# Kernel optimization log

Measured on AMD Instinct MI355X. Metric: run time of the kernel, lower is better.

The kernel has to match this reference:

```python
import jax, jax.numpy as jnp
import numpy as np

LN_EPS = 1e-5


def _layer_norm(x, scale, bias):
    mu = jnp.mean(x, axis=-1, keepdims=True)
    var = jnp.mean(jnp.square(x - mu), axis=-1, keepdims=True)
    return (x - mu) * jax.lax.rsqrt(var + LN_EPS) * scale + bias


def setup_inputs() -> dict:
    key = jax.random.key(0)
    B, N, C_Z, C_H = 1, 512, 128, 128
    ks = jax.random.split(key, 8)
    s = 1.0 / np.sqrt(C_Z)
    inp = {
        "z": jax.random.normal(ks[0], (B, N, N, C_Z), dtype=jnp.float32),
        "mask": jnp.ones((B, N, N), dtype=jnp.float32),
        # gated / plain projections from c_z -> c_hidden
        "w_a_p": jax.random.normal(ks[1], (C_Z, C_H), dtype=jnp.float32) * s,
        "b_a_p": jnp.zeros((C_H,), dtype=jnp.float32),
        "w_a_g": jnp.zeros((C_Z, C_H), dtype=jnp.float32),  # gating init: zeros, bias ones
        "b_a_g": jnp.ones((C_H,), dtype=jnp.float32),
        "w_b_p": jax.random.normal(ks[2], (C_Z, C_H), dtype=jnp.float32) * s,
        "b_b_p": jnp.zeros((C_H,), dtype=jnp.float32),
        "w_b_g": jnp.zeros((C_Z, C_H), dtype=jnp.float32),
        "b_b_g": jnp.ones((C_H,), dtype=jnp.float32),
        # output gate c_z -> c_z (gating init)
        "w_g": jnp.zeros((C_Z, C_Z), dtype=jnp.float32),
        "b_g": jnp.ones((C_Z,), dtype=jnp.float32),
        # final projection c_hidden -> c_z ('final' init: zeros; use small randn for a nontrivial test)
        "w_z": jax.random.normal(ks[3], (C_H, C_Z), dtype=jnp.float32) * (1.0 / np.sqrt(C_H)),
        "b_z": jnp.zeros((C_Z,), dtype=jnp.float32),
        "ln_in_scale": jnp.ones((C_Z,), dtype=jnp.float32),
        "ln_in_bias": jnp.zeros((C_Z,), dtype=jnp.float32),
        "ln_out_scale": jnp.ones((C_H,), dtype=jnp.float32),
        "ln_out_bias": jnp.zeros((C_H,), dtype=jnp.float32),
    }
    return inp


def reference(z, mask, w_a_p, b_a_p, w_a_g, b_a_g, w_b_p, b_b_p, w_b_g, b_b_g,
              w_g, b_g, w_z, b_z, ln_in_scale, ln_in_bias, ln_out_scale, ln_out_bias):
    # tmu_type == 'outgoing'
    z = _layer_norm(z, ln_in_scale, ln_in_bias)          # [B,N,N,Cz]
    m = mask[..., None]                                   # [B,N,N,1]
    a = jax.nn.sigmoid(z @ w_a_g + b_a_g) * m * (z @ w_a_p + b_a_p)  # [B,N,N,Ch]
    b = jax.nn.sigmoid(z @ w_b_g + b_b_g) * m * (z @ w_b_p + b_b_p)  # [B,N,N,Ch]
    # outgoing: p[b,i,j,c] = sum_k a[b,i,k,c] * b[b,j,k,c]
    x = jnp.einsum("bikc,bjkc->bijc", a, b)              # [B,N,N,Ch]
    x = _layer_norm(x, ln_out_scale, ln_out_bias)
    x = x @ w_z + b_z                                    # [B,N,N,Cz]
    g = jax.nn.sigmoid(z @ w_g + b_g)                    # [B,N,N,Cz]
    return x * g
```

## Files before the change

### kernel.cpp

```cpp
#include <hip/hip_runtime.h>

typedef __attribute__((ext_vector_type(8))) short short8;
typedef __attribute__((ext_vector_type(4))) short short4v;
typedef __attribute__((ext_vector_type(4))) float float4v;
typedef __attribute__((ext_vector_type(2))) unsigned int uint2v;

#define NDIM 512
#define NN (NDIM*NDIM)
#define CD 128

__device__ __forceinline__ unsigned short f2b(float f) {
  union { float f; unsigned u; } v; v.f = f;
  unsigned r = v.u + 0x7FFFu + ((v.u >> 16) & 1u);
  return (unsigned short)(r >> 16);
}
__device__ __forceinline__ float b2f(unsigned short h) {
  union { unsigned u; float f; } v; v.u = ((unsigned)h) << 16; return v.f;
}
__device__ __forceinline__ float sigmoidf_(float x) { return 1.f / (1.f + __expf(-x)); }
__device__ __forceinline__ unsigned pk2(float a, float b) {
  return (unsigned)f2b(a) | ((unsigned)f2b(b) << 16);
}
__device__ __forceinline__ float4v mfma16(short8 a, short8 b, float4v c) {
  return __builtin_amdgcn_mfma_f32_16x16x32_bf16(a, b, c, 0, 0, 0);
}
__device__ __forceinline__ void gl_lds16(const short* g, short* l) {
  __builtin_amdgcn_global_load_lds(
      (const __attribute__((address_space(1))) unsigned int*)g,
      (__attribute__((address_space(3))) unsigned int*)l, 16, 0, 0);
}

__device__ __forceinline__ short8 fragr(const short* buf, int row, int j) {
  return *(const short8*)(buf + row * 128 + ((j ^ (row & 15)) << 3));
}

__device__ __forceinline__ void stageW(const short* wslot, short* sW, int t) {
#pragma unroll
  for (int i = 0; i < 8; ++i) {
    int U = i * 256 + t;
    int row = U >> 4, u = U & 15;
    gl_lds16(wslot + row * 128 + ((u ^ (row & 15)) << 3), sW + U * 8);
  }
}

__global__ __launch_bounds__(256) void kPrepW(
    const float* __restrict__ w0, const float* __restrict__ w1,
    const float* __restrict__ w2, const float* __restrict__ w3,
    const float* __restrict__ w4, short* __restrict__ wt)
{
  const int wi = blockIdx.y;
  const float* W = wi==0 ? w0 : wi==1 ? w1 : wi==2 ? w2 : wi==3 ? w3 : w4;
  const int e = blockIdx.x * 256 + threadIdx.x;
  const int k = e >> 7, n = e & 127;
  wt[wi * 16384 + n * 128 + k] = (short)f2b(W[k * CD + n]);
}

__global__ __launch_bounds__(256, 2) void kProj(
    const float* __restrict__ z, const float* __restrict__ mask,
    const short* __restrict__ wT,
    const float* __restrict__ b_a_p, const float* __restrict__ b_a_g,
    const float* __restrict__ b_b_p, const float* __restrict__ b_b_g,
    const float* __restrict__ b_g,
    const float* __restrict__ ln_s, const float* __restrict__ ln_b,
    short* __restrict__ a_t, short* __restrict__ b_t, short* __restrict__ g_out)
{
  __shared__ short zln[128 * 128];
  __shared__ short sW[128 * 128];
  const int t = threadIdx.x;
  const int r0 = blockIdx.x * 128;
  const int w = t >> 6, l = t & 63, lr = l & 15, lg = l >> 4;

  stageW(wT + 1 * 16384, sW, t);

#pragma unroll
  for (int h = 0; h < 2; ++h) {
    const int row = h * 64 + (t >> 2), q = t & 3;
    const float* zp = z + (size_t)(r0 + row) * CD + q * 32;
    float x[32];
#pragma unroll
    for (int i = 0; i < 8; ++i) {
      float4v v = *(const float4v*)(zp + i * 4);
#pragma unroll
      for (int e = 0; e < 4; ++e) x[i*4+e] = v[e];
    }
    float s = 0.f;
#pragma unroll
    for (int i = 0; i < 32; ++i) s += x[i];
    s += __shfl_xor(s, 1, 64);
    s += __shfl_xor(s, 2, 64);
    const float mu = s * (1.f/128.f);
    float vs = 0.f;
#pragma unroll
    for (int i = 0; i < 32; ++i) { float d = x[i]-mu; vs += d*d; }
    vs += __shfl_xor(vs, 1, 64);
    vs += __shfl_xor(vs, 2, 64);
    const float rstd = rsqrtf(vs * (1.f/128.f) + 1e-5f);
#pragma unroll
    for (int i = 0; i < 32; ++i) {
      int c = q*32 + i;
      float y = (x[i]-mu)*rstd*ln_s[c] + ln_b[c];
      zln[row*128 + (((c>>3) ^ (row & 15)) << 3) + (c & 7)] = (short)f2b(y);
    }
  }

  float bga[8], bpa[8], bgb[8], bpb[8];
#pragma unroll
  for (int cf = 0; cf < 8; ++cf) {
    bga[cf] = b_a_g[cf*16+lr]; bpa[cf] = b_a_p[cf*16+lr];
    bgb[cf] = b_b_g[cf*16+lr]; bpb[cf] = b_b_p[cf*16+lr];
  }
  float mrow[2][4];
#pragma unroll
  for (int g = 0; g < 2; ++g)
#pragma unroll
    for (int jj = 0; jj < 4; ++jj)
      mrow[g][jj] = mask[r0 + w*32 + g*16 + lg*4 + jj];

  __syncthreads();

  short8 af[2][4];
#pragma unroll
  for (int g = 0; g < 2; ++g)
#pragma unroll
    for (int ks = 0; ks < 4; ++ks)
      af[g][ks] = fragr(zln, w*32 + g*16 + lr, ks*4 + lg);

  float4v accA[2][8], accB[2][8];
  float sg[2][8][4];

#define ZERO_ACC(A) do { _Pragma("unroll") for (int g_=0;g_<2;++g_) \
  _Pragma("unroll") for (int c_=0;c_<8;++c_) A[g_][c_] = (float4v){0.f,0.f,0.f,0.f}; } while(0)

#define WPASS(A) do { ZERO_ACC(A);                                         \
  _Pragma("unroll") for (int ks_=0; ks_<4; ++ks_)                          \
    _Pragma("unroll") for (int cf_=0; cf_<8; ++cf_) {                      \
      short8 wf_ = fragr(sW, cf_*16 + lr, ks_*4 + lg);                     \
      _Pragma("unroll") for (int g_=0; g_<2; ++g_)                         \
        A[g_][cf_] = mfma16(af[g_][ks_], wf_, A[g_][cf_]);                 \
    } } while(0)

#define SIGPASS(BG) do { _Pragma("unroll") for (int g_=0;g_<2;++g_)        \
  _Pragma("unroll") for (int cf_=0;cf_<8;++cf_)                            \
    _Pragma("unroll") for (int j_=0;j_<4;++j_)                             \
      sg[g_][cf_][j_] = sigmoidf_(accA[g_][cf_][j_] + BG[cf_]) * mrow[g_][j_]; } while(0)

#define STORE_AB(DST, BP) do { _Pragma("unroll") for (int g_=0;g_<2;++g_)  \
  _Pragma("unroll") for (int cf_=0;cf_<8;++cf_) {                          \
    float v0_ = sg[g_][cf_][0] * (accB[g_][cf_][0] + BP[cf_]);             \
    float v1_ = sg[g_][cf_][1] * (accB[g_][cf_][1] + BP[cf_]);             \
    float v2_ = sg[g_][cf_][2] * (accB[g_][cf_][2] + BP[cf_]);             \
    float v3_ = sg[g_][cf_][3] * (accB[g_][cf_][3] + BP[cf_]);             \
    uint2v pv_ = { pk2(v0_, v1_), pk2(v2_, v3_) };                         \
    *(uint2v*)(DST + (size_t)(cf_*16+lr)*NN + r0 + w*32 + g_*16 + lg*4) = pv_; \
  } } while(0)

  WPASS(accA);
  SIGPASS(bga);
  __syncthreads();
  stageW(wT + 0 * 16384, sW, t);
  __syncthreads();
  WPASS(accB);
  __syncthreads();
  stageW(wT + 3 * 16384, sW, t);
  STORE_AB(a_t, bpa);
  __syncthreads();
  WPASS(accA);
  SIGPASS(bgb);
  __syncthreads();
  stageW(wT + 2 * 16384, sW, t);
  __syncthreads();
  WPASS(accB);
  __syncthreads();
  stageW(wT + 4 * 16384, sW, t);
  STORE_AB(b_t, bpb);
  __syncthreads();
  {
    float4v accG[2][8];
    ZERO_ACC(accG);
#pragma unroll
    for (int ks = 0; ks < 4; ++ks)
#pragma unroll
      for (int cf = 0; cf < 8; ++cf) {
        short8 wf = fragr(sW, cf*16 + lr, ks*4 + lg);
#pragma unroll
        for (int g = 0; g < 2; ++g)
          accG[g][cf] = mfma16(wf, af[g][ks], accG[g][cf]);
      }
#pragma unroll
    for (int g = 0; g < 2; ++g)
#pragma unroll
      for (int cf = 0; cf < 8; ++cf) {
        float4v bgv = *(const float4v*)(b_g + cf*16 + lg*4);
        float v0 = sigmoidf_(accG[g][cf][0] + bgv[0]);
        float v1 = sigmoidf_(accG[g][cf][1] + bgv[1]);
        float v2 = sigmoidf_(accG[g][cf][2] + bgv[2]);
        float v3 = sigmoidf_(accG[g][cf][3] + bgv[3]);
        uint2v pv = { pk2(v0, v1), pk2(v2, v3) };
        *(uint2v*)(g_out + (size_t)(r0 + w*32 + g*16 + lr)*CD + cf*16 + lg*4) = pv;
      }
  }
}

__global__ __launch_bounds__(256, 2) void kEinsum(const short* __restrict__ a_t,
                                                  const short* __restrict__ b_t,
                                                  short* __restrict__ x_t)
{
  __shared__ short As[2][128 * 64];
  __shared__ short Bs[2][128 * 64];
  const int t = threadIdx.x;
  const int d = blockIdx.x;
  const int c = (d & 7) * 16 + (d >> 7);
  const int tile = (d >> 3) & 15;
  const int i0 = (tile >> 2) * 128;
  const int j0 = (tile & 3) * 128;
  const size_t abase = (size_t)c * NN;
  const int w = t >> 6, l = t & 63, lr = l & 15, lg = l >> 4;
  const int wr = w >> 1, wc = w & 1;

  const short* gA[4]; const short* gB[4]; int ldsU[4];
#pragma unroll
  for (int q = 0; q < 4; ++q) {
    int U = q * 256 + t;
    int row = U >> 3, u = U & 7;
    int swz = ((u ^ (row & 7)) << 3);
    gA[q] = a_t + abase + (size_t)(i0 + row) * NDIM + swz;
    gB[q] = b_t + abase + (size_t)(j0 + row) * NDIM + swz;
    ldsU[q] = U * 8;
  }

#define STAGE_E(buf, k0) do { _Pragma("unroll") for (int q_=0;q_<4;++q_) { \
    gl_lds16(gA[q_] + (k0), &As[buf][ldsU[q_]]);                           \
    gl_lds16(gB[q_] + (k0), &Bs[buf][ldsU[q_]]); } } while(0)

  float4v acc[4][4];
#pragma unroll
  for (int m = 0; m < 4; ++m)
#pragma unroll
    for (int n = 0; n < 4; ++n) acc[m][n] = (float4v){0.f,0.f,0.f,0.f};

  STAGE_E(0, 0);
  __syncthreads();
  int cur = 0;
#pragma unroll
  for (int it = 0; it < 8; ++it) {
    if (it < 7) STAGE_E(cur ^ 1, (it + 1) * 64);
    short8 afr[4][2], bfr[4][2];
#pragma unroll
    for (int m = 0; m < 4; ++m)
#pragma unroll
      for (int ks = 0; ks < 2; ++ks) {
        int row = wr*64 + m*16 + lr, j = ks*4 + lg;
        afr[m][ks] = *(const short8*)(&As[cur][row*64 + ((j ^ (row & 7)) << 3)]);
      }
#pragma unroll
    for (int n = 0; n < 4; ++n)
#pragma unroll
      for (int ks = 0; ks < 2; ++ks) {
        int row = wc*64 + n*16 + lr, j = ks*4 + lg;
        bfr[n][ks] = *(const short8*)(&Bs[cur][row*64 + ((j ^ (row & 7)) << 3)]);
      }
#pragma unroll
    for (int ks = 0; ks < 2; ++ks)
#pragma unroll
      for (int m = 0; m < 4; ++m)
#pragma unroll
        for (int n = 0; n < 4; ++n)
          acc[m][n] = mfma16(bfr[n][ks], afr[m][ks], acc[m][n]);
    __syncthreads();
    cur ^= 1;
  }
#pragma unroll
  for (int m = 0; m < 4; ++m)
#pragma unroll
    for (int n = 0; n < 4; ++n) {
      int i  = i0 + wr*64 + m*16 + lr;
      int jb = j0 + wc*64 + n*16 + lg*4;
      uint2v pv = { pk2(acc[m][n][0], acc[m][n][1]), pk2(acc[m][n][2], acc[m][n][3]) };
      *(uint2v*)(x_t + abase + (size_t)i * NDIM + jb) = pv;
    }
}

__global__ __launch_bounds__(256, 2) void kOut(
    const short* __restrict__ x_t, const short* __restrict__ g_in,
    const float* __restrict__ w_z, const float* __restrict__ b_z,
    const float* __restrict__ ln_s, const float* __restrict__ ln_b,
    float* __restrict__ out)
{
  __shared__ short xs[128 * 72];
  __shared__ short xln[64 * 128];
  __shared__ short sW[128 * 128];
  const int t = threadIdx.x;
  const int r0 = blockIdx.x * 64;
  const int w = t >> 6, l = t & 63, lr = l & 15, lg = l >> 4;

#pragma unroll
  for (int i = 0; i < 8; ++i) {
    int flat = i * 256 + t;
    int kp = flat >> 5, k = kp * 2, n4 = (flat & 31) * 4;
    float4v va = *(const float4v*)(w_z + (size_t)k * CD + n4);
    float4v vb = *(const float4v*)(w_z + (size_t)(k + 1) * CD + n4);
#pragma unroll
    for (int j = 0; j < 4; ++j) {
      int row = n4 + j;
      int addr = row * 128 + (((k >> 3) ^ (row & 15)) << 3) + (k & 7);
      *(unsigned*)(&sW[addr]) = pk2(va[j], vb[j]);
    }
  }
#pragma unroll
  for (int it = 0; it < 4; ++it) {
    int v = it * 256 + t; int cc = v >> 3; int u = v & 7;
    int up = u ^ ((cc >> 3) & 7);
    *(short8*)&xs[cc * 72 + up * 8] = *(const short8*)(x_t + (size_t)cc * NN + r0 + u * 8);
  }
  __syncthreads();
  {
    const int r = t >> 2, q = t & 3;
    float x[32];
#pragma unroll
    for (int i = 0; i < 32; ++i) {
      int c = q * 32 + i;
      x[i] = b2f((unsigned short)xs[c * 72 + (((r >> 3) ^ ((c >> 3) & 7)) << 3) + (r & 7)]);
    }
    float s = 0.f;
#pragma unroll
    for (int i = 0; i < 32; ++i) s += x[i];
    s += __shfl_xor(s, 1, 64);
    s += __shfl_xor(s, 2, 64);
    const float mu = s * (1.f/128.f);
    float vs = 0.f;
#pragma unroll
    for (int i = 0; i < 32; ++i) { float d = x[i]-mu; vs += d*d; }
    vs += __shfl_xor(vs, 1, 64);
    vs += __shfl_xor(vs, 2, 64);
    const float rstd = rsqrtf(vs * (1.f/128.f) + 1e-5f);
#pragma unroll
    for (int i = 0; i < 32; ++i) {
      int c = q*32 + i;
      float y = (x[i]-mu)*rstd*ln_s[c] + ln_b[c];
      xln[r*128 + (((c>>3) ^ (r & 15)) << 3) + (c & 7)] = (short)f2b(y);
    }
  }
  __syncthreads();
  short8 af[4];
#pragma unroll
  for (int ks = 0; ks < 4; ++ks)
    af[ks] = fragr(xln, w*16 + lr, ks*4 + lg);

  float4v acc[8];
#pragma unroll
  for (int cf = 0; cf < 8; ++cf) acc[cf] = (float4v){0.f,0.f,0.f,0.f};
#pragma unroll
  for (int ks = 0; ks < 4; ++ks)
#pragma unroll
    for (int cf = 0; cf < 8; ++cf) {
      short8 wf = fragr(sW, cf*16 + lr, ks*4 + lg);
      acc[cf] = mfma16(wf, af[ks], acc[cf]);
    }
  const int orow = r0 + w*16 + lr;
#pragma unroll
  for (int cf = 0; cf < 8; ++cf) {
    float4v bzv = *(const float4v*)(b_z + cf*16 + lg*4);
    short4v gv = *(const short4v*)(g_in + (size_t)orow * CD + cf*16 + lg*4);
    float4v o;
#pragma unroll
    for (int j = 0; j < 4; ++j)
      o[j] = (acc[cf][j] + bzv[j]) * b2f((unsigned short)gv[j]);
    *(float4v*)(out + (size_t)orow * CD + cf*16 + lg*4) = o;
  }
}

extern "C" void kernel_launch(void* const* d_in, const int* in_sizes, int n_in,
                              void* d_out, int out_size, void* d_ws, size_t ws_size,
                              hipStream_t stream) {
  (void)in_sizes; (void)n_in; (void)out_size; (void)ws_size;
  const float* z     = (const float*)d_in[0];
  const float* mask  = (const float*)d_in[1];
  const float* w_a_p = (const float*)d_in[2];
  const float* b_a_p = (const float*)d_in[3];
  const float* w_a_g = (const float*)d_in[4];
  const float* b_a_g = (const float*)d_in[5];
  const float* w_b_p = (const float*)d_in[6];
  const float* b_b_p = (const float*)d_in[7];
  const float* w_b_g = (const float*)d_in[8];
  const float* b_b_g = (const float*)d_in[9];
  const float* w_g   = (const float*)d_in[10];
  const float* b_g   = (const float*)d_in[11];
  const float* w_z   = (const float*)d_in[12];
  const float* b_z   = (const float*)d_in[13];
  const float* ln_i_s = (const float*)d_in[14];
  const float* ln_i_b = (const float*)d_in[15];
  const float* ln_o_s = (const float*)d_in[16];
  const float* ln_o_b = (const float*)d_in[17];

  short* a_t = (short*)d_ws;
  short* b_t = a_t + (size_t)CD*NN;
  short* g_s = b_t + (size_t)CD*NN;
  short* x_t = g_s + (size_t)CD*NN;
  short* wT  = x_t;

  hipLaunchKernelGGL(kPrepW, dim3(64, 5), dim3(256), 0, stream,
                     w_a_p, w_a_g, w_b_p, w_b_g, w_g, wT);
  hipLaunchKernelGGL(kProj, dim3(NN/128), dim3(256), 0, stream,
                     z, mask, wT, b_a_p, b_a_g, b_b_p, b_b_g, b_g,
                     ln_i_s, ln_i_b, a_t, b_t, g_s);
  hipLaunchKernelGGL(kEinsum, dim3(2048), dim3(256), 0, stream, a_t, b_t, x_t);
  hipLaunchKernelGGL(kOut, dim3(NN/64), dim3(256), 0, stream,
                     x_t, g_s, w_z, b_z, ln_o_s, ln_o_b, (float*)d_out);
}
```

Baseline: 366.0 us.

## Double-buffer weight staging in projection kernel and use hardware bf16 pack

Once the A fragments are held in registers, the LN'd z tile's LDS buffer is reused as a second weight buffer. This lets the next weight matrix load asynchronously while the current MFMA pass runs, and removes about half the barriers in kProj. The float-to-bf16 packing now uses the v_cvt_pk_bf16_f32 instruction instead of software rounding, and LN output stores are paired into 32-bit writes. s_setprio raises wave priority around MFMA loops in kProj and kEinsum. The cost is tighter ordering between LDS reuse and barriers, and possibly different rounding behaviour from the hardware convert.

```diff
diff --git a/kernel.cpp b/kernel.cpp
--- a/kernel.cpp
+++ b/kernel.cpp
@@ -19,7 +19,9 @@
 }
 __device__ __forceinline__ float sigmoidf_(float x) { return 1.f / (1.f + __expf(-x)); }
 __device__ __forceinline__ unsigned pk2(float a, float b) {
-  return (unsigned)f2b(a) | ((unsigned)f2b(b) << 16);
+  unsigned r;
+  asm("v_cvt_pk_bf16_f32 %0, %1, %2" : "=v"(r) : "v"(a), "v"(b));
+  return r;
 }
 __device__ __forceinline__ float4v mfma16(short8 a, short8 b, float4v c) {
   return __builtin_amdgcn_mfma_f32_16x16x32_bf16(a, b, c, 0, 0, 0);
@@ -32,15 +34,6 @@
 
 __device__ __forceinline__ short8 fragr(const short* buf, int row, int j) {
   return *(const short8*)(buf + row * 128 + ((j ^ (row & 15)) << 3));
-}
-
-__device__ __forceinline__ void stageW(const short* wslot, short* sW, int t) {
-#pragma unroll
-  for (int i = 0; i < 8; ++i) {
-    int U = i * 256 + t;
-    int row = U >> 4, u = U & 15;
-    gl_lds16(wslot + row * 128 + ((u ^ (row & 15)) << 3), sW + U * 8);
-  }
 }
 
 __global__ __launch_bounds__(256) void kPrepW(
@@ -70,7 +63,18 @@
   const int r0 = blockIdx.x * 128;
   const int w = t >> 6, l = t & 63, lr = l & 15, lg = l >> 4;
 
-  stageW(wT + 1 * 16384, sW, t);
+  int soff[8], doff[8];
+#pragma unroll
+  for (int i = 0; i < 8; ++i) {
+    int U = i * 256 + t;
+    int row = U >> 4, u = U & 15;
+    soff[i] = row * 128 + ((u ^ (row & 15)) << 3);
+    doff[i] = U * 8;
+  }
+#define STAGE(BUF, SLOT) do { _Pragma("unroll") for (int i_ = 0; i_ < 8; ++i_) \
+    gl_lds16(wT + (SLOT) * 16384 + soff[i_], (BUF) + doff[i_]); } while(0)
+
+  STAGE(sW, 1);
 
 #pragma unroll
   for (int h = 0; h < 2; ++h) {
@@ -96,10 +100,12 @@
     vs += __shfl_xor(vs, 2, 64);
     const float rstd = rsqrtf(vs * (1.f/128.f) + 1e-5f);
 #pragma unroll
-    for (int i = 0; i < 32; ++i) {
+    for (int i = 0; i < 32; i += 2) {
       int c = q*32 + i;
-      float y = (x[i]-mu)*rstd*ln_s[c] + ln_b[c];
-      zln[row*128 + (((c>>3) ^ (row & 15)) << 3) + (c & 7)] = (short)f2b(y);
+      float y0 = (x[i]  -mu)*rstd*ln_s[c]   + ln_b[c];
+      float y1 = (x[i+1]-mu)*rstd*ln_s[c+1] + ln_b[c+1];
+      int addr = row*128 + (((c>>3) ^ (row & 15)) << 3) + (c & 7);
+      *(unsigned*)(&zln[addr]) = pk2(y0, y1);
     }
   }
 
@@ -124,6 +130,7 @@
 #pragma unroll
     for (int ks = 0; ks < 4; ++ks)
       af[g][ks] = fragr(zln, w*32 + g*16 + lr, ks*4 + lg);
+  __syncthreads();
 
   float4v accA[2][8], accB[2][8];
   float sg[2][8][4];
@@ -131,13 +138,15 @@
 #define ZERO_ACC(A) do { _Pragma("unroll") for (int g_=0;g_<2;++g_) \
   _Pragma("unroll") for (int c_=0;c_<8;++c_) A[g_][c_] = (float4v){0.f,0.f,0.f,0.f}; } while(0)
 
-#define WPASS(A) do { ZERO_ACC(A);                                         \
+#define WPASS(A, BUF) do { ZERO_ACC(A);                                    \
+  __builtin_amdgcn_s_setprio(1);                                           \
   _Pragma("unroll") for (int ks_=0; ks_<4; ++ks_)                          \
     _Pragma("unroll") for (int cf_=0; cf_<8; ++cf_) {                      \
-      short8 wf_ = fragr(sW, cf_*16 + lr, ks_*4 + lg);                     \
+      short8 wf_ = fragr(BUF, cf_*16 + lr, ks_*4 + lg);                    \
       _Pragma("unroll") for (int g_=0; g_<2; ++g_)                         \
         A[g_][cf_] = mfma16(af[g_][ks_], wf_, A[g_][cf_]);                 \
-    } } while(0)
+    }                                                                      \
+  __builtin_amdgcn_s_setprio(0); } while(0)
 
 #define SIGPASS(BG) do { _Pragma("unroll") for (int g_=0;g_<2;++g_)        \
   _Pragma("unroll") for (int cf_=0;cf_<8;++cf_)                            \
@@ -154,29 +163,26 @@
     *(uint2v*)(DST + (size_t)(cf_*16+lr)*NN + r0 + w*32 + g_*16 + lg*4) = pv_; \
   } } while(0)
 
-  WPASS(accA);
+  STAGE(zln, 0);
+  WPASS(accA, sW);
+  __syncthreads();
+  STAGE(sW, 3);
+  WPASS(accB, zln);
   SIGPASS(bga);
   __syncthreads();
-  stageW(wT + 0 * 16384, sW, t);
-  __syncthreads();
-  WPASS(accB);
-  __syncthreads();
-  stageW(wT + 3 * 16384, sW, t);
+  STAGE(zln, 2);
+  WPASS(accA, sW);
   STORE_AB(a_t, bpa);
   __syncthreads();
-  WPASS(accA);
+  STAGE(sW, 4);
+  WPASS(accB, zln);
   SIGPASS(bgb);
   __syncthreads();
-  stageW(wT + 2 * 16384, sW, t);
-  __syncthreads();
-  WPASS(accB);
-  __syncthreads();
-  stageW(wT + 4 * 16384, sW, t);
-  STORE_AB(b_t, bpb);
-  __syncthreads();
+
   {
     float4v accG[2][8];
     ZERO_ACC(accG);
+    __builtin_amdgcn_s_setprio(1);
 #pragma unroll
     for (int ks = 0; ks < 4; ++ks)
 #pragma unroll
@@ -186,6 +192,8 @@
         for (int g = 0; g < 2; ++g)
           accG[g][cf] = mfma16(wf, af[g][ks], accG[g][cf]);
       }
+    __builtin_amdgcn_s_setprio(0);
+    STORE_AB(b_t, bpb);
 #pragma unroll
     for (int g = 0; g < 2; ++g)
 #pragma unroll
@@ -259,6 +267,7 @@
         int row = wc*64 + n*16 + lr, j = ks*4 + lg;
         bfr[n][ks] = *(const short8*)(&Bs[cur][row*64 + ((j ^ (row & 7)) << 3)]);
       }
+    __builtin_amdgcn_s_setprio(1);
 #pragma unroll
     for (int ks = 0; ks < 2; ++ks)
 #pragma unroll
@@ -266,6 +275,7 @@
 #pragma unroll
         for (int n = 0; n < 4; ++n)
           acc[m][n] = mfma16(bfr[n][ks], afr[m][ks], acc[m][n]);
+    __builtin_amdgcn_s_setprio(0);
     __syncthreads();
     cur ^= 1;
   }
```

Result: no change. 369.4 us (+0.9%).
